# Performance work log

Hardware: AMD Instinct MI355X
Metric: run time of the kernel (lower is better)

## Reference

```python
import jax, jax.numpy as jnp
import numpy as np

B, N, D, H, L = 2, 2048, 512, 8, 2
HD = D // H


def setup_inputs() -> dict:
    key = jax.random.key(0)
    ks = jax.random.split(key, 8)
    s = 0.02
    return {
        "inputs_embeds": jax.random.normal(ks[0], (B, N, D), jnp.float32),
        "pos_emb": jax.random.normal(ks[1], (N, D), jnp.float32) * s,
        "c_attn_w": jax.random.normal(ks[2], (L, D, 3 * D), jnp.float32) * s,
        "c_attn_b": jnp.zeros((L, 3 * D), jnp.float32),
        "out_w": jax.random.normal(ks[3], (L, D, D), jnp.float32) * s,
        "out_b": jnp.zeros((L, D), jnp.float32),
        "ln1_g": jnp.ones((L, D), jnp.float32),
        "ln1_b": jnp.zeros((L, D), jnp.float32),
        "c_fc_w": jax.random.normal(ks[4], (L, D, 4 * D), jnp.float32) * s,
        "c_fc_b": jnp.zeros((L, 4 * D), jnp.float32),
        "c_proj_w": jax.random.normal(ks[5], (L, 4 * D, D), jnp.float32) * s,
        "c_proj_b": jnp.zeros((L, D), jnp.float32),
        "ln2_g": jnp.ones((L, D), jnp.float32),
        "ln2_b": jnp.zeros((L, D), jnp.float32),
    }


def _layernorm(x, g, b, eps=1e-5):
    mu = jnp.mean(x, axis=-1, keepdims=True)
    var = jnp.mean(jnp.square(x - mu), axis=-1, keepdims=True)
    return (x - mu) * jax.lax.rsqrt(var + eps) * g + b


def _gelu_new(x):
    # NewGELUActivation: tanh approximation
    return 0.5 * x * (1.0 + jnp.tanh(jnp.sqrt(2.0 / jnp.pi) * (x + 0.044715 * x ** 3)))


def _attention(x, w_qkv, b_qkv, w_out, b_out, self_mask):
    qkv = x @ w_qkv + b_qkv                      # [B,N,3D]
    q, k, v = jnp.split(qkv, 3, axis=-1)
    def heads(t):
        return t.reshape(B, N, H, HD).transpose(0, 2, 1, 3)  # [B,H,N,HD]
    q, k, v = heads(q), heads(k), heads(v)
    scores = jnp.einsum('bhqd,bhkd->bhqk', q, k) / jnp.sqrt(jnp.float32(HD))
    neg = jnp.finfo(scores.dtype).min
    scores = jnp.where(self_mask, scores, neg)   # exclude-self mask
    attn = jax.nn.softmax(scores, axis=-1)
    o = jnp.einsum('bhqk,bhkd->bhqd', attn, v)
    o = o.transpose(0, 2, 1, 3).reshape(B, N, D)
    return o @ w_out + b_out


def reference(inputs_embeds, pos_emb, c_attn_w, c_attn_b, out_w, out_b,
              ln1_g, ln1_b, c_fc_w, c_fc_b, c_proj_w, c_proj_b, ln2_g, ln2_b):
    self_mask = ~jnp.eye(N, dtype=bool)[None, None]  # [1,1,N,N]
    h = inputs_embeds + pos_emb[None]
    for l in range(L):
        res = h
        x = _layernorm(h, ln1_g[l], ln1_b[l])
        h = _attention(x, c_attn_w[l], c_attn_b[l], out_w[l], out_b[l], self_mask) + res
        res = h
        x = _layernorm(h, ln2_g[l], ln2_b[l])
        x = _gelu_new(x @ c_fc_w[l] + c_fc_b[l])
        h = (x @ c_proj_w[l] + c_proj_b[l]) + res
    return h
```

## Files before the change

### kernel.cpp

```cpp
#include <hip/hip_runtime.h>
#include <hip/hip_bf16.h>
#include <math.h>

#define BB 2
#define NN 2048
#define DD 512
#define HH 8
#define LL 2
#define TT (BB*NN)

typedef short short8 __attribute__((ext_vector_type(8)));
typedef float floatx4 __attribute__((ext_vector_type(4)));

__device__ __forceinline__ unsigned short f2b(float v) {
    union { float f; unsigned u; } x; x.f = v;
    unsigned r = x.u + 0x7fff + ((x.u >> 16) & 1);
    return (unsigned short)(r >> 16);
}

__global__ __launch_bounds__(256) void k_embed(const float* __restrict__ emb,
                                               const float* __restrict__ pos,
                                               float* __restrict__ h) {
    int i = blockIdx.x * 256 + threadIdx.x;
    h[i] = emb[i] + pos[i & (NN * DD - 1)];
}

__global__ __launch_bounds__(256) void k_bias_add(const float* __restrict__ src,
                                                  const float* __restrict__ bias,
                                                  float* __restrict__ dst) {
    int i = blockIdx.x * 256 + threadIdx.x;
    dst[i] = src[i] + bias[i & (DD - 1)];
}

__global__ __launch_bounds__(256) void k_ln(const float* __restrict__ hin,
                                            unsigned short* __restrict__ xout,
                                            const float* __restrict__ g,
                                            const float* __restrict__ b) {
    __shared__ float red[4];
    __shared__ float bc1, bc2;
    int t = blockIdx.x;
    int tid = threadIdx.x;
    int lane = tid & 63, wv = tid >> 6;
    const float* row = hin + (size_t)t * DD;
    float v0 = row[tid];
    float v1 = row[tid + 256];

    float s = v0 + v1;
#pragma unroll
    for (int o = 32; o; o >>= 1) s += __shfl_down(s, o, 64);
    if (lane == 0) red[wv] = s;
    __syncthreads();
    if (tid == 0) bc1 = (red[0] + red[1] + red[2] + red[3]) * (1.0f / DD);
    __syncthreads();
    float mu = bc1;
    float d0 = v0 - mu, d1 = v1 - mu;
    s = d0 * d0 + d1 * d1;
#pragma unroll
    for (int o = 32; o; o >>= 1) s += __shfl_down(s, o, 64);
    if (lane == 0) red[wv] = s;
    __syncthreads();
    if (tid == 0) bc2 = (red[0] + red[1] + red[2] + red[3]) * (1.0f / DD);
    __syncthreads();
    float rstd = rsqrtf(bc2 + 1e-5f);
    xout[(size_t)t * DD + tid]       = f2b(d0 * rstd * g[tid] + b[tid]);
    xout[(size_t)t * DD + tid + 256] = f2b(d1 * rstd * g[tid + 256] + b[tid + 256]);
}

__device__ __forceinline__ float gelu_new(float v) {
    const float c = 0.7978845608028654f;
    float u = c * (v + 0.044715f * v * v * v);
    return 0.5f * v * (1.0f + tanhf(u));
}

#define PL 3145728
__global__ __launch_bounds__(256) void k_wt_all(const float* __restrict__ c_attn_w,
                                                const float* __restrict__ out_w,
                                                const float* __restrict__ c_fc_w,
                                                const float* __restrict__ c_proj_w,
                                                unsigned short* __restrict__ wbuf) {
    __shared__ unsigned short t[64][72];
    int bx = blockIdx.x;
    int l = bx / 768;
    int r = bx - l * 768;
    const float* W; unsigned short* WT; int K, N;
    if (r < 192)      { W = c_attn_w + (size_t)l * 512 * 1536; WT = wbuf + (size_t)l * PL;           K = 512;  N = 1536; }
    else if (r < 256) { r -= 192; W = out_w  + (size_t)l * 512 * 512;  WT = wbuf + (size_t)l * PL + 786432;  K = 512;  N = 512; }
    else if (r < 512) { r -= 256; W = c_fc_w + (size_t)l * 512 * 2048; WT = wbuf + (size_t)l * PL + 1048576; K = 512;  N = 2048; }
    else              { r -= 512; W = c_proj_w + (size_t)l * 2048 * 512; WT = wbuf + (size_t)l * PL + 2097152; K = 2048; N = 512; }
    int tiles_n = N >> 6;
    int n0 = (r % tiles_n) * 64, k0 = (r / tiles_n) * 64;

    int tid = threadIdx.x;
    int rr = tid >> 2;
    int c0 = (tid & 3) * 16;
    const float* src = W + (size_t)(k0 + rr) * N + n0 + c0;
#pragma unroll
    for (int u = 0; u < 4; u++) {
        float4 v = *(const float4*)&src[u * 4];
        t[c0 + u * 4 + 0][rr] = f2b(v.x);
        t[c0 + u * 4 + 1][rr] = f2b(v.y);
        t[c0 + u * 4 + 2][rr] = f2b(v.z);
        t[c0 + u * 4 + 3][rr] = f2b(v.w);
    }
    __syncthreads();
    unsigned short* dst = WT + (size_t)(n0 + rr) * K + k0 + c0;
#pragma unroll
    for (int u = 0; u < 4; u++)
        *(uint2*)&dst[u * 4] = *(const uint2*)&t[rr][c0 + u * 4];
}

template <int ACT, int RES, int BF16OUT, int ATOMIC>
__global__ __launch_bounds__(256) void k_mgemm(const unsigned short* __restrict__ Ab,
                                               const unsigned short* __restrict__ Bt,
                                               const float* __restrict__ bias,
                                               const float* __restrict__ Rp,
                                               float* __restrict__ Cp,
                                               unsigned short* __restrict__ Cb,
                                               int Kfull, int Kchunk, int N) {
    __shared__ unsigned short Als[8 * 512];
    __shared__ unsigned short Bls[8 * 512];

    int tid = threadIdx.x;
    int l = tid & 63, w = tid >> 6;
    int wm = w >> 1, wn = w & 1;
    int m0 = blockIdx.y * 128, n0 = blockIdx.x * 128;
    int kb = blockIdx.z * Kchunk;
    int lr = l & 15;
    int lk = (l >> 4) * 8;

    const unsigned short* Ap0 = Ab + (size_t)(m0 + (w * 2 + 0) * 16 + lr) * Kfull + kb + lk;
    const unsigned short* Ap1 = Ab + (size_t)(m0 + (w * 2 + 1) * 16 + lr) * Kfull + kb + lk;
    const unsigned short* Bp0 = Bt + (size_t)(n0 + (w * 2 + 0) * 16 + lr) * Kfull + kb + lk;
    const unsigned short* Bp1 = Bt + (size_t)(n0 + (w * 2 + 1) * 16 + lr) * Kfull + kb + lk;

    floatx4 acc[4][4];
#pragma unroll
    for (int i = 0; i < 4; i++)
#pragma unroll
        for (int j = 0; j < 4; j++) acc[i][j] = (floatx4){0.f, 0.f, 0.f, 0.f};

    uint4 ra0 = *(const uint4*)Ap0;
    uint4 ra1 = *(const uint4*)Ap1;
    uint4 rb0 = *(const uint4*)Bp0;
    uint4 rb1 = *(const uint4*)Bp1;

    for (int k0 = 0; k0 < Kchunk; k0 += 32) {
        __syncthreads();
        *(uint4*)&Als[(w * 2 + 0) * 512 + l * 8] = ra0;
        *(uint4*)&Als[(w * 2 + 1) * 512 + l * 8] = ra1;
        *(uint4*)&Bls[(w * 2 + 0) * 512 + l * 8] = rb0;
        *(uint4*)&Bls[(w * 2 + 1) * 512 + l * 8] = rb1;
        __syncthreads();
        if (k0 + 32 < Kchunk) {
            ra0 = *(const uint4*)(Ap0 + k0 + 32);
            ra1 = *(const uint4*)(Ap1 + k0 + 32);
            rb0 = *(const uint4*)(Bp0 + k0 + 32);
            rb1 = *(const uint4*)(Bp1 + k0 + 32);
        }
        short8 a[4], b[4];
#pragma unroll
        for (int i = 0; i < 4; i++) {
            a[i] = *(const short8*)&Als[(wm * 4 + i) * 512 + l * 8];
            b[i] = *(const short8*)&Bls[(wn * 4 + i) * 512 + l * 8];
        }
#pragma unroll
        for (int i = 0; i < 4; i++)
#pragma unroll
            for (int j = 0; j < 4; j++)
                acc[i][j] = __builtin_amdgcn_mfma_f32_16x16x32_bf16(a[i], b[j], acc[i][j], 0, 0, 0);
    }

    int col_in = l & 15, rquad = (l >> 4) * 4;
#pragma unroll
    for (int i = 0; i < 4; i++) {
        int gm_base = m0 + wm * 64 + i * 16 + rquad;
#pragma unroll
        for (int j = 0; j < 4; j++) {
            int gn = n0 + wn * 64 + j * 16 + col_in;
            float bv = ATOMIC ? 0.0f : bias[gn];
#pragma unroll
            for (int r = 0; r < 4; r++) {
                size_t off = (size_t)(gm_base + r) * N + gn;
                if (ATOMIC) {
                    atomicAdd(&Cp[off], acc[i][j][r]);
                } else {
                    float v = acc[i][j][r] + bv;
                    if (ACT) v = gelu_new(v);
                    if (RES) v += Rp[off];
                    if (BF16OUT) Cb[off] = f2b(v);
                    else Cp[off] = v;
                }
            }
        }
    }
}

__global__ __launch_bounds__(256) void k_attn_mfma(const unsigned short* __restrict__ qkv,
                                                   unsigned short* __restrict__ xatt) {
    __shared__ unsigned short Ks[64 * 72];
    __shared__ unsigned short Vt[64 * 72];
    __shared__ unsigned short Pls[64 * 72];

    int qt = blockIdx.x, hd = blockIdx.y, b = blockIdx.z;
    int tid = threadIdx.x;
    int l = tid & 63, w = tid >> 6;
    int lr = l & 15, quad = l >> 4;

    const size_t base = (size_t)b * NN * 1536;

    short8 qf[2];
    {
        const unsigned short* qrow = qkv + base + (size_t)(qt * 64 + w * 16 + lr) * 1536 + hd * 64;
        qf[0] = *(const short8*)&qrow[quad * 8];
        qf[1] = *(const short8*)&qrow[quad * 8 + 32];
    }

    floatx4 O[4];
#pragma unroll
    for (int jd = 0; jd < 4; jd++) O[jd] = (floatx4){0.f, 0.f, 0.f, 0.f};
    float lsum = 0.0f;

    int sr = tid >> 2, sc = (tid & 3) * 16;
    int vk = (tid & 15) * 4, vd = (tid >> 4) * 4;
    const unsigned short* Kbase = qkv + base + 512 + hd * 64;
    const unsigned short* Vbase = qkv + base + 1024 + hd * 64;

    uint4 rk0, rk1;
    union { uint2 u; unsigned short s[4]; } rv[4];
    rk0 = *(const uint4*)&Kbase[(size_t)sr * 1536 + sc];
    rk1 = *(const uint4*)&Kbase[(size_t)sr * 1536 + sc + 8];
#pragma unroll
    for (int i = 0; i < 4; i++)
        rv[i].u = *(const uint2*)&Vbase[(size_t)(vk + i) * 1536 + vd];

    for (int kt = 0; kt < 32; kt++) {
        __syncthreads();
        *(uint4*)&Ks[sr * 72 + sc]     = rk0;
        *(uint4*)&Ks[sr * 72 + sc + 8] = rk1;
#pragma unroll
        for (int j = 0; j < 4; j++) {
            union { uint2 u; unsigned short s[4]; } pk;
            pk.s[0] = rv[0].s[j]; pk.s[1] = rv[1].s[j];
            pk.s[2] = rv[2].s[j]; pk.s[3] = rv[3].s[j];
            *(uint2*)&Vt[(vd + j) * 72 + vk] = pk.u;
        }
        __syncthreads();
        if (kt < 31) {
            int kn = (kt + 1) * 64;
            rk0 = *(const uint4*)&Kbase[(size_t)(kn + sr) * 1536 + sc];
            rk1 = *(const uint4*)&Kbase[(size_t)(kn + sr) * 1536 + sc + 8];
#pragma unroll
            for (int i = 0; i < 4; i++)
                rv[i].u = *(const uint2*)&Vbase[(size_t)(kn + vk + i) * 1536 + vd];
        }

        floatx4 s[4];
#pragma unroll
        for (int jn = 0; jn < 4; jn++) s[jn] = (floatx4){0.f, 0.f, 0.f, 0.f};
#pragma unroll
        for (int ss = 0; ss < 2; ss++)
#pragma unroll
            for (int jn = 0; jn < 4; jn++) {
                short8 ak = *(const short8*)&Ks[(jn * 16 + lr) * 72 + ss * 32 + quad * 8];
                s[jn] = __builtin_amdgcn_mfma_f32_16x16x32_bf16(ak, qf[ss], s[jn], 0, 0, 0);
            }

        int mq = w * 16 + lr;
#pragma unroll
        for (int jn = 0; jn < 4; jn++) {
            union { uint2 u; unsigned short h[4]; } pk;
#pragma unroll
            for (int r = 0; r < 4; r++) {
                float p = __expf(s[jn][r] * 0.125f - 8.0f);
                if (kt == qt && mq == jn * 16 + quad * 4 + r) p = 0.0f;
                lsum += p;
                pk.h[r] = f2b(p);
            }
            *(uint2*)&Pls[mq * 72 + jn * 16 + quad * 4] = pk.u;
        }

#pragma unroll
        for (int ss = 0; ss < 2; ss++) {
            short8 ap = *(const short8*)&Pls[(w * 16 + lr) * 72 + ss * 32 + quad * 8];
#pragma unroll
            for (int jd = 0; jd < 4; jd++) {
                short8 bv = *(const short8*)&Vt[(jd * 16 + lr) * 72 + ss * 32 + quad * 8];
                O[jd] = __builtin_amdgcn_mfma_f32_16x16x32_bf16(ap, bv, O[jd], 0, 0, 0);
            }
        }
    }

    lsum += __shfl_xor(lsum, 16);
    lsum += __shfl_xor(lsum, 32);
#pragma unroll
    for (int r = 0; r < 4; r++) {
        float inv = 1.0f / __shfl(lsum, quad * 4 + r, 16);
        size_t tok = (size_t)b * NN + qt * 64 + w * 16 + quad * 4 + r;
#pragma unroll
        for (int jd = 0; jd < 4; jd++)
            xatt[tok * DD + hd * 64 + jd * 16 + lr] = f2b(O[jd][r] * inv);
    }
}

extern "C" void kernel_launch(void* const* d_in, const int* in_sizes, int n_in,
                              void* d_out, int out_size, void* d_ws, size_t ws_size,
                              hipStream_t stream) {
    const float* emb      = (const float*)d_in[0];
    const float* pos      = (const float*)d_in[1];
    const float* c_attn_w = (const float*)d_in[2];
    const float* c_attn_b = (const float*)d_in[3];
    const float* out_w    = (const float*)d_in[4];
    const float* out_b    = (const float*)d_in[5];
    const float* ln1_g    = (const float*)d_in[6];
    const float* ln1_b    = (const float*)d_in[7];
    const float* c_fc_w   = (const float*)d_in[8];
    const float* c_fc_b   = (const float*)d_in[9];
    const float* c_proj_w = (const float*)d_in[10];
    const float* c_proj_b = (const float*)d_in[11];
    const float* ln2_g    = (const float*)d_in[12];
    const float* ln2_b    = (const float*)d_in[13];

    char* p = (char*)d_ws;
    float* h = (float*)p;                       p += (size_t)TT * DD * 4;
    unsigned short* act = (unsigned short*)p;   p += (size_t)TT * 2048 * 2;
    unsigned short* x = (unsigned short*)p;     p += (size_t)TT * DD * 2;
    unsigned short* xatt = (unsigned short*)p;  p += (size_t)TT * DD * 2;
    unsigned short* wbuf = (unsigned short*)p;

    unsigned short* qkvb = act;
    unsigned short* ffa  = act;
    float* out = (float*)d_out;

    k_embed<<<TT * DD / 256, 256, 0, stream>>>(emb, pos, h);
    k_wt_all<<<1536, 256, 0, stream>>>(c_attn_w, out_w, c_fc_w, c_proj_w, wbuf);

    for (int l = 0; l < LL; l++) {
        unsigned short* wqkv_t  = wbuf + (size_t)l * PL;
        unsigned short* wout_t  = wqkv_t + 786432;
        unsigned short* wfc_t   = wqkv_t + 1048576;
        unsigned short* wproj_t = wqkv_t + 2097152;
        float* proj_dst = (l == LL - 1) ? out : h;

        k_ln<<<TT, 256, 0, stream>>>(h, x, ln1_g + l * DD, ln1_b + l * DD);
        k_mgemm<0, 0, 1, 0><<<dim3(1536 / 128, TT / 128), 256, 0, stream>>>(
            x, wqkv_t, c_attn_b + l * 1536, nullptr, nullptr, qkvb, 512, 512, 1536);
        k_attn_mfma<<<dim3(NN / 64, HH, BB), 256, 0, stream>>>(qkvb, xatt);
        k_bias_add<<<TT * DD / 256, 256, 0, stream>>>(h, out_b + l * DD, h);
        k_mgemm<0, 0, 0, 1><<<dim3(512 / 128, TT / 128, 2), 256, 0, stream>>>(
            xatt, wout_t, nullptr, nullptr, h, nullptr, 512, 256, 512);
        k_ln<<<TT, 256, 0, stream>>>(h, x, ln2_g + l * DD, ln2_b + l * DD);
        k_mgemm<1, 0, 1, 0><<<dim3(2048 / 128, TT / 128), 256, 0, stream>>>(
            x, wfc_t, c_fc_b + l * 2048, nullptr, nullptr, ffa, 512, 512, 2048);
        k_bias_add<<<TT * DD / 256, 256, 0, stream>>>(h, c_proj_b + l * DD, proj_dst);
        k_mgemm<0, 0, 0, 1><<<dim3(512 / 128, TT / 128, 4), 256, 0, stream>>>(
            ffa, wproj_t, nullptr, nullptr, proj_dst, nullptr, 2048, 512, 512);
    }
}
```

Measured before the change: 450.3 us.

## Double-buffer GEMM and attention LDS, fold bias into atomics, MFMA row sums

The GEMM and attention kernels now use double-buffered LDS tiles so each iteration has one barrier instead of two, and global prefetch runs two stages ahead. The attention softmax uses exp2 with a pre-folded scale constant and truncating bf16 packing. Row sums are computed by an extra MFMA against a ones vector instead of scalar accumulation and shuffles. Separate bias-add kernels are removed by adding the bias in the z=0 split of the atomic GEMMs. The changes double shared memory use, which may reduce occupancy, and the bf16 truncation slightly changes rounding.

```diff
diff --git a/kernel.cpp b/kernel.cpp
--- a/kernel.cpp
+++ b/kernel.cpp
@@ -16,6 +16,18 @@
     union { float f; unsigned u; } x; x.f = v;
     unsigned r = x.u + 0x7fff + ((x.u >> 16) & 1);
     return (unsigned short)(r >> 16);
+}
+
+__device__ __forceinline__ unsigned fbits(float v) {
+    union { float f; unsigned u; } x; x.f = v; return x.u;
+}
+
+__device__ __forceinline__ unsigned pk_bf16_rtz(float a, float b) {
+#if __has_builtin(__builtin_amdgcn_perm)
+    return __builtin_amdgcn_perm(fbits(b), fbits(a), 0x07060302);
+#else
+    return (fbits(b) & 0xFFFF0000u) | (fbits(a) >> 16);
+#endif
 }
 
 __global__ __launch_bounds__(256) void k_embed(const float* __restrict__ emb,
@@ -109,16 +121,15 @@
         *(uint2*)&dst[u * 4] = *(const uint2*)&t[rr][c0 + u * 4];
 }
 
-template <int ACT, int RES, int BF16OUT, int ATOMIC>
+template <int ACT, int BF16OUT, int ATOMIC>
 __global__ __launch_bounds__(256) void k_mgemm(const unsigned short* __restrict__ Ab,
                                                const unsigned short* __restrict__ Bt,
                                                const float* __restrict__ bias,
-                                               const float* __restrict__ Rp,
                                                float* __restrict__ Cp,
                                                unsigned short* __restrict__ Cb,
                                                int Kfull, int Kchunk, int N) {
-    __shared__ unsigned short Als[8 * 512];
-    __shared__ unsigned short Bls[8 * 512];
+    __shared__ unsigned short Als[2][8 * 512];
+    __shared__ unsigned short Bls[2][8 * 512];
 
     int tid = threadIdx.x;
     int l = tid & 63, w = tid >> 6;
@@ -132,61 +143,79 @@
     const unsigned short* Ap1 = Ab + (size_t)(m0 + (w * 2 + 1) * 16 + lr) * Kfull + kb + lk;
     const unsigned short* Bp0 = Bt + (size_t)(n0 + (w * 2 + 0) * 16 + lr) * Kfull + kb + lk;
     const unsigned short* Bp1 = Bt + (size_t)(n0 + (w * 2 + 1) * 16 + lr) * Kfull + kb + lk;
+    int la0 = (w * 2 + 0) * 512 + l * 8;
+    int la1 = (w * 2 + 1) * 512 + l * 8;
 
     floatx4 acc[4][4];
 #pragma unroll
     for (int i = 0; i < 4; i++)
 #pragma unroll
         for (int j = 0; j < 4; j++) acc[i][j] = (floatx4){0.f, 0.f, 0.f, 0.f};
+
+    int nit = Kchunk >> 5;
 
     uint4 ra0 = *(const uint4*)Ap0;
     uint4 ra1 = *(const uint4*)Ap1;
     uint4 rb0 = *(const uint4*)Bp0;
     uint4 rb1 = *(const uint4*)Bp1;
-
-    for (int k0 = 0; k0 < Kchunk; k0 += 32) {
-        __syncthreads();
-        *(uint4*)&Als[(w * 2 + 0) * 512 + l * 8] = ra0;
-        *(uint4*)&Als[(w * 2 + 1) * 512 + l * 8] = ra1;
-        *(uint4*)&Bls[(w * 2 + 0) * 512 + l * 8] = rb0;
-        *(uint4*)&Bls[(w * 2 + 1) * 512 + l * 8] = rb1;
-        __syncthreads();
-        if (k0 + 32 < Kchunk) {
-            ra0 = *(const uint4*)(Ap0 + k0 + 32);
-            ra1 = *(const uint4*)(Ap1 + k0 + 32);
-            rb0 = *(const uint4*)(Bp0 + k0 + 32);
-            rb1 = *(const uint4*)(Bp1 + k0 + 32);
+    *(uint4*)&Als[0][la0] = ra0;
+    *(uint4*)&Als[0][la1] = ra1;
+    *(uint4*)&Bls[0][la0] = rb0;
+    *(uint4*)&Bls[0][la1] = rb1;
+    if (nit > 1) {
+        ra0 = *(const uint4*)(Ap0 + 32);
+        ra1 = *(const uint4*)(Ap1 + 32);
+        rb0 = *(const uint4*)(Bp0 + 32);
+        rb1 = *(const uint4*)(Bp1 + 32);
+    }
+    __syncthreads();
+
+    for (int it = 0; it < nit; it++) {
+        int c = it & 1;
+        if (it + 1 < nit) {
+            *(uint4*)&Als[c ^ 1][la0] = ra0;
+            *(uint4*)&Als[c ^ 1][la1] = ra1;
+            *(uint4*)&Bls[c ^ 1][la0] = rb0;
+            *(uint4*)&Bls[c ^ 1][la1] = rb1;
+        }
+        if (it + 2 < nit) {
+            int ko = (it + 2) << 5;
+            ra0 = *(const uint4*)(Ap0 + ko);
+            ra1 = *(const uint4*)(Ap1 + ko);
+            rb0 = *(const uint4*)(Bp0 + ko);
+            rb1 = *(const uint4*)(Bp1 + ko);
         }
         short8 a[4], b[4];
 #pragma unroll
         for (int i = 0; i < 4; i++) {
-            a[i] = *(const short8*)&Als[(wm * 4 + i) * 512 + l * 8];
-            b[i] = *(const short8*)&Bls[(wn * 4 + i) * 512 + l * 8];
+            a[i] = *(const short8*)&Als[c][(wm * 4 + i) * 512 + l * 8];
+            b[i] = *(const short8*)&Bls[c][(wn * 4 + i) * 512 + l * 8];
         }
 #pragma unroll
         for (int i = 0; i < 4; i++)
 #pragma unroll
             for (int j = 0; j < 4; j++)
                 acc[i][j] = __builtin_amdgcn_mfma_f32_16x16x32_bf16(a[i], b[j], acc[i][j], 0, 0, 0);
+        __syncthreads();
     }
 
     int col_in = l & 15, rquad = (l >> 4) * 4;
+    bool addb = (!ATOMIC) || (bias != nullptr && blockIdx.z == 0);
 #pragma unroll
     for (int i = 0; i < 4; i++) {
         int gm_base = m0 + wm * 64 + i * 16 + rquad;
 #pragma unroll
         for (int j = 0; j < 4; j++) {
             int gn = n0 + wn * 64 + j * 16 + col_in;
-            float bv = ATOMIC ? 0.0f : bias[gn];
+            float bv = addb ? bias[gn] : 0.0f;
 #pragma unroll
             for (int r = 0; r < 4; r++) {
                 size_t off = (size_t)(gm_base + r) * N + gn;
                 if (ATOMIC) {
-                    atomicAdd(&Cp[off], acc[i][j][r]);
+                    atomicAdd(&Cp[off], acc[i][j][r] + bv);
                 } else {
                     float v = acc[i][j][r] + bv;
                     if (ACT) v = gelu_new(v);
-                    if (RES) v += Rp[off];
                     if (BF16OUT) Cb[off] = f2b(v);
                     else Cp[off] = v;
                 }
@@ -197,8 +226,8 @@
 
 __global__ __launch_bounds__(256) void k_attn_mfma(const unsigned short* __restrict__ qkv,
                                                    unsigned short* __restrict__ xatt) {
-    __shared__ unsigned short Ks[64 * 72];
-    __shared__ unsigned short Vt[64 * 72];
+    __shared__ unsigned short Ks[2][64 * 72];
+    __shared__ unsigned short Vt[2][64 * 72];
     __shared__ unsigned short Pls[64 * 72];
 
     int qt = blockIdx.x, hd = blockIdx.y, b = blockIdx.z;
@@ -214,39 +243,63 @@
         qf[0] = *(const short8*)&qrow[quad * 8];
         qf[1] = *(const short8*)&qrow[quad * 8 + 32];
     }
+    short8 onef;
+#pragma unroll
+    for (int i = 0; i < 8; i++) onef[i] = (short)0x3F80;
 
     floatx4 O[4];
 #pragma unroll
     for (int jd = 0; jd < 4; jd++) O[jd] = (floatx4){0.f, 0.f, 0.f, 0.f};
-    float lsum = 0.0f;
+    floatx4 sacc = (floatx4){0.f, 0.f, 0.f, 0.f};
 
     int sr = tid >> 2, sc = (tid & 3) * 16;
     int vk = (tid & 15) * 4, vd = (tid >> 4) * 4;
     const unsigned short* Kbase = qkv + base + 512 + hd * 64;
     const unsigned short* Vbase = qkv + base + 1024 + hd * 64;
 
-    uint4 rk0, rk1;
+    uint4 rk0 = *(const uint4*)&Kbase[(size_t)sr * 1536 + sc];
+    uint4 rk1 = *(const uint4*)&Kbase[(size_t)sr * 1536 + sc + 8];
     union { uint2 u; unsigned short s[4]; } rv[4];
-    rk0 = *(const uint4*)&Kbase[(size_t)sr * 1536 + sc];
-    rk1 = *(const uint4*)&Kbase[(size_t)sr * 1536 + sc + 8];
 #pragma unroll
     for (int i = 0; i < 4; i++)
         rv[i].u = *(const uint2*)&Vbase[(size_t)(vk + i) * 1536 + vd];
+    *(uint4*)&Ks[0][sr * 72 + sc]     = rk0;
+    *(uint4*)&Ks[0][sr * 72 + sc + 8] = rk1;
+#pragma unroll
+    for (int j = 0; j < 4; j++) {
+        union { uint2 u; unsigned short s[4]; } pk;
+        pk.s[0] = rv[0].s[j]; pk.s[1] = rv[1].s[j];
+        pk.s[2] = rv[2].s[j]; pk.s[3] = rv[3].s[j];
+        *(uint2*)&Vt[0][(vd + j) * 72 + vk] = pk.u;
+    }
+    {
+        rk0 = *(const uint4*)&Kbase[(size_t)(64 + sr) * 1536 + sc];
+        rk1 = *(const uint4*)&Kbase[(size_t)(64 + sr) * 1536 + sc + 8];
+#pragma unroll
+        for (int i = 0; i < 4; i++)
+            rv[i].u = *(const uint2*)&Vbase[(size_t)(64 + vk + i) * 1536 + vd];
+    }
+    __syncthreads();
+
+    const float C1 = 0.18033688f;
+    const float C2 = -11.5415603f;
+    int mq = w * 16 + lr;
 
     for (int kt = 0; kt < 32; kt++) {
-        __syncthreads();
-        *(uint4*)&Ks[sr * 72 + sc]     = rk0;
-        *(uint4*)&Ks[sr * 72 + sc + 8] = rk1;
-#pragma unroll
-        for (int j = 0; j < 4; j++) {
-            union { uint2 u; unsigned short s[4]; } pk;
-            pk.s[0] = rv[0].s[j]; pk.s[1] = rv[1].s[j];
-            pk.s[2] = rv[2].s[j]; pk.s[3] = rv[3].s[j];
-            *(uint2*)&Vt[(vd + j) * 72 + vk] = pk.u;
-        }
-        __syncthreads();
+        int c = kt & 1;
         if (kt < 31) {
-            int kn = (kt + 1) * 64;
+            *(uint4*)&Ks[c ^ 1][sr * 72 + sc]     = rk0;
+            *(uint4*)&Ks[c ^ 1][sr * 72 + sc + 8] = rk1;
+#pragma unroll
+            for (int j = 0; j < 4; j++) {
+                union { uint2 u; unsigned short s[4]; } pk;
+                pk.s[0] = rv[0].s[j]; pk.s[1] = rv[1].s[j];
+                pk.s[2] = rv[2].s[j]; pk.s[3] = rv[3].s[j];
+                *(uint2*)&Vt[c ^ 1][(vd + j) * 72 + vk] = pk.u;
+            }
+        }
+        if (kt < 30) {
+            int kn = (kt + 2) * 64;
             rk0 = *(const uint4*)&Kbase[(size_t)(kn + sr) * 1536 + sc];
             rk1 = *(const uint4*)&Kbase[(size_t)(kn + sr) * 1536 + sc + 8];
 #pragma unroll
@@ -261,22 +314,22 @@
         for (int ss = 0; ss < 2; ss++)
 #pragma unroll
             for (int jn = 0; jn < 4; jn++) {
-                short8 ak = *(const short8*)&Ks[(jn * 16 + lr) * 72 + ss * 32 + quad * 8];
+                short8 ak = *(const short8*)&Ks[c][(jn * 16 + lr) * 72 + ss * 32 + quad * 8];
                 s[jn] = __builtin_amdgcn_mfma_f32_16x16x32_bf16(ak, qf[ss], s[jn], 0, 0, 0);
             }
 
-        int mq = w * 16 + lr;
 #pragma unroll
         for (int jn = 0; jn < 4; jn++) {
-            union { uint2 u; unsigned short h[4]; } pk;
+            float p[4];
 #pragma unroll
             for (int r = 0; r < 4; r++) {
-                float p = __expf(s[jn][r] * 0.125f - 8.0f);
-                if (kt == qt && mq == jn * 16 + quad * 4 + r) p = 0.0f;
-                lsum += p;
-                pk.h[r] = f2b(p);
+                p[r] = exp2f(fmaf(s[jn][r], C1, C2));
+                if (kt == qt && mq == jn * 16 + quad * 4 + r) p[r] = 0.0f;
             }
-            *(uint2*)&Pls[mq * 72 + jn * 16 + quad * 4] = pk.u;
+            uint2 pk;
+            pk.x = pk_bf16_rtz(p[0], p[1]);
+            pk.y = pk_bf16_rtz(p[2], p[3]);
+            *(uint2*)&Pls[mq * 72 + jn * 16 + quad * 4] = pk;
         }
 
 #pragma unroll
@@ -284,17 +337,17 @@
             short8 ap = *(const short8*)&Pls[(w * 16 + lr) * 72 + ss * 32 + quad * 8];
 #pragma unroll
             for (int jd = 0; jd < 4; jd++) {
-                short8 bv = *(const short8*)&Vt[(jd * 16 + lr) * 72 + ss * 32 + quad * 8];
+                short8 bv = *(const short8*)&Vt[c][(jd * 16 + lr) * 72 + ss * 32 + quad * 8];
                 O[jd] = __builtin_amdgcn_mfma_f32_16x16x32_bf16(ap, bv, O[jd], 0, 0, 0);
             }
-        }
-    }
-
-    lsum += __shfl_xor(lsum, 16);
-    lsum += __shfl_xor(lsum, 32);
+            sacc = __builtin_amdgcn_mfma_f32_16x16x32_bf16(ap, onef, sacc, 0, 0, 0);
+        }
+        __syncthreads();
+    }
+
 #pragma unroll
     for (int r = 0; r < 4; r++) {
-        float inv = 1.0f / __shfl(lsum, quad * 4 + r, 16);
+        float inv = 1.0f / sacc[r];
         size_t tok = (size_t)b * NN + qt * 64 + w * 16 + quad * 4 + r;
 #pragma unroll
         for (int jd = 0; jd < 4; jd++)
@@ -339,20 +392,23 @@
         unsigned short* wout_t  = wqkv_t + 786432;
         unsigned short* wfc_t   = wqkv_t + 1048576;
         unsigned short* wproj_t = wqkv_t + 2097152;
-        float* proj_dst = (l == LL - 1) ? out : h;
 
         k_ln<<<TT, 256, 0, stream>>>(h, x, ln1_g + l * DD, ln1_b + l * DD);
-        k_mgemm<0, 0, 1, 0><<<dim3(1536 / 128, TT / 128), 256, 0, stream>>>(
-            x, wqkv_t, c_attn_b + l * 1536, nullptr, nullptr, qkvb, 512, 512, 1536);
+        k_mgemm<0, 1, 0><<<dim3(1536 / 128, TT / 128), 256, 0, stream>>>(
+            x, wqkv_t, c_attn_b + l * 1536, nullptr, qkvb, 512, 512, 1536);
         k_attn_mfma<<<dim3(NN / 64, HH, BB), 256, 0, stream>>>(qkvb, xatt);
-        k_bias_add<<<TT * DD / 256, 256, 0, stream>>>(h, out_b + l * DD, h);
-        k_mgemm<0, 0, 0, 1><<<dim3(512 / 128, TT / 128, 2), 256, 0, stream>>>(
-            xatt, wout_t, nullptr, nullptr, h, nullptr, 512, 256, 512);
+        k_mgemm<0, 0, 1><<<dim3(512 / 128, TT / 128, 2), 256, 0, stream>>>(
+            xatt, wout_t, out_b + l * DD, h, nullptr, 512, 256, 512);
         k_ln<<<TT, 256, 0, stream>>>(h, x, ln2_g + l * DD, ln2_b + l * DD);
-        k_mgemm<1, 0, 1, 0><<<dim3(2048 / 128, TT / 128), 256, 0, stream>>>(
-            x, wfc_t, c_fc_b + l * 2048, nullptr, nullptr, ffa, 512, 512, 2048);
-        k_bias_add<<<TT * DD / 256, 256, 0, stream>>>(h, c_proj_b + l * DD, proj_dst);
-        k_mgemm<0, 0, 0, 1><<<dim3(512 / 128, TT / 128, 4), 256, 0, stream>>>(
-            ffa, wproj_t, nullptr, nullptr, proj_dst, nullptr, 2048, 512, 512);
-    }
-}
+        k_mgemm<1, 1, 0><<<dim3(2048 / 128, TT / 128), 256, 0, stream>>>(
+            x, wfc_t, c_fc_b + l * 2048, nullptr, ffa, 512, 512, 2048);
+        if (l == LL - 1) {
+            k_bias_add<<<TT * DD / 256, 256, 0, stream>>>(h, c_proj_b + l * DD, out);
+            k_mgemm<0, 0, 1><<<dim3(512 / 128, TT / 128, 4), 256, 0, stream>>>(
+                ffa, wproj_t, nullptr, out, nullptr, 2048, 512, 512);
+        } else {
+            k_mgemm<0, 0, 1><<<dim3(512 / 128, TT / 128, 4), 256, 0, stream>>>(
+                ffa, wproj_t, c_proj_b + l * DD, h, nullptr, 2048, 512, 512);
+        }
+    }
+}
```

Measured after the change: 442.5 us. Within noise of the previous version (-1.7%).
